# Optimization experiments

Measured on AMD Instinct MI355X. Metric: run time of the kernel, lower is better.

Reference implementation:

```python
import math
import jax, jax.numpy as jnp
import numpy as np

I_DIM = 64
N_MODES = 16
FACTOR = 4
EPS = 1e-5


def group_norm(x, w, b):
    # x: [B, M, N, C] channels-last; torch GroupNorm(C//16, C) over (group_channels, M, N)
    B, M, N, C = x.shape
    g = C // 16
    xr = x.reshape(B, M, N, g, C // g)
    mean = xr.mean(axis=(1, 2, 4), keepdims=True)
    var = xr.var(axis=(1, 2, 4), keepdims=True)
    xr = (xr - mean) * jax.lax.rsqrt(var + EPS)
    return xr.reshape(B, M, N, C) * w + b


def feed_forward(x, res, l1w, l1b, l2w, l2b, g1w, g1b, g2w, g2b, g3w, g3b):
    h = x @ l1w + l1b                      # [B,M,N,C*factor]
    h = group_norm(h, g1w, g1b)            # fork_1
    h = jax.nn.relu(h)
    h = h @ l2w + l2b                      # [B,M,N,C]
    h = group_norm(h, g2w, g2b)            # fork_2
    h = res + h
    h = group_norm(h, g3w, g3b)            # fork_3
    return h


def setup_inputs() -> dict:
    key = jax.random.key(0)
    ks = jax.random.split(key, 20)
    B, M, N, I = 4, 128, 128, I_DIM
    H = I * FACTOR
    z = jax.random.normal(ks[0], (B, 2 * M * N * I, 1), dtype=jnp.float32)
    x = jax.random.normal(ks[1], (B, M * N * I, 1), dtype=jnp.float32)
    # fourier weights [in, out, nm, nm, 2], xavier-ish scale
    fw_scale = math.sqrt(2.0 / (I + I))
    fw1 = jax.random.normal(ks[2], (I, I, N_MODES, N_MODES, 2), dtype=jnp.float32) * fw_scale
    fw2 = jax.random.normal(ks[3], (I, I, N_MODES, N_MODES, 2), dtype=jnp.float32) * fw_scale
    def ff_params(k0):
        kk = jax.random.split(k0, 4)
        return dict(
            l1w=jax.random.normal(kk[0], (I, H), dtype=jnp.float32) * math.sqrt(2.0 / (I + H)),
            l1b=jnp.zeros((H,), jnp.float32),
            l2w=jax.random.normal(kk[1], (H, I), dtype=jnp.float32) * math.sqrt(2.0 / (I + H)),
            l2b=jnp.zeros((I,), jnp.float32),
            g1w=jnp.ones((H,), jnp.float32), g1b=jnp.zeros((H,), jnp.float32),
            g2w=jnp.ones((I,), jnp.float32), g2b=jnp.zeros((I,), jnp.float32),
            g3w=jnp.ones((I,), jnp.float32), g3b=jnp.zeros((I,), jnp.float32),
        )
    bp = ff_params(ks[4])
    fp = ff_params(ks[5])
    out = {"z": z, "x": x, "fw1": fw1, "fw2": fw2}
    for name, p in (("b", bp), ("f", fp)):
        for k, v in p.items():
            out[f"{name}_{k}"] = v
    return out


def reference(z, x, fw1, fw2,
              b_l1w, b_l1b, b_l2w, b_l2b, b_g1w, b_g1b, b_g2w, b_g2b, b_g3w, b_g3b,
              f_l1w, f_l1b, f_l2w, f_l2b, f_g1w, f_g1b, f_g2w, f_g2b, f_g3w, f_g3b):
    I = I_DIM
    nm = N_MODES
    B = x.shape[0]
    M = N = int(math.sqrt(x.shape[1] // I))
    x4 = x.reshape(B, M, N, I)
    z5 = z.reshape(B, 2, M, N, I)
    backcast, forecast = z5[:, 0], z5[:, 1]
    x4 = x4 - backcast
    xc = jnp.transpose(x4, (0, 3, 1, 2))          # [B, I, M, N]
    x_ft = jnp.fft.rfft2(xc, s=(M, N), norm='ortho')  # [B, I, M, N//2+1] complex64
    w1 = fw1[..., 0] + 1j * fw1[..., 1]
    w2 = fw2[..., 0] + 1j * fw2[..., 1]
    top = jnp.einsum('bixy,ioxy->boxy', x_ft[:, :, :nm, :nm], w1)
    bot = jnp.einsum('bixy,ioxy->boxy', x_ft[:, :, -nm:, :nm], w2)
    out_ft = jnp.zeros((B, I, N, M // 2 + 1), dtype=x_ft.dtype)
    out_ft = out_ft.at[:, :, :nm, :nm].set(top).at[:, :, -nm:, :nm].set(bot)
    xo = jnp.fft.irfft2(out_ft, s=(N, M), norm='ortho')  # [B, I, M, N]
    xo = jnp.transpose(xo, (0, 2, 3, 1))                  # [B, M, N, I]
    backcast = feed_forward(xo, backcast, b_l1w, b_l1b, b_l2w, b_l2b,
                            b_g1w, b_g1b, b_g2w, b_g2b, b_g3w, b_g3b)
    forecast = feed_forward(xo, forecast, f_l1w, f_l1b, f_l2w, f_l2b,
                            f_g1w, f_g1b, f_g2w, f_g2b, f_g3w, f_g3b)
    out = jnp.stack([backcast, forecast], axis=1)         # [B, 2, M, N, I]
    return out.reshape(B, 2 * M * N * I, 1)
```

## Files before the change

kernel.cpp:

```cpp
#include <hip/hip_runtime.h>
#include <hip/hip_bf16.h>

typedef __hip_bfloat16 bf16;
typedef __attribute__((ext_vector_type(8))) short short8;
typedef __attribute__((ext_vector_type(4))) float f32x4;

#define PI2 6.283185307179586f
#define EPSV 1e-5f

__device__ __forceinline__ short f2bs(float f){
  bf16 h = __float2bfloat16(f);
  short s; __builtin_memcpy(&s, &h, 2); return s;
}
__device__ __forceinline__ float s2f(short s){
  bf16 h; __builtin_memcpy(&h, &s, 2); return __bfloat162float(h);
}
__device__ __forceinline__ float4 f4add(float4 a, float4 b){ return make_float4(a.x+b.x, a.y+b.y, a.z+b.z, a.w+b.w); }
__device__ __forceinline__ float4 f4sub(float4 a, float4 b){ return make_float4(a.x-b.x, a.y-b.y, a.z-b.z, a.w-b.w); }

__global__ __launch_bounds__(256) void k_prep_ydft(
    const float* __restrict__ x, const float* __restrict__ z,
    const float* __restrict__ fw1, const float* __restrict__ fw2,
    float2* __restrict__ FWT,
    const float* __restrict__ b_l1w, const float* __restrict__ b_l1b,
    const float* __restrict__ b_l2w, const float* __restrict__ b_l2b,
    const float* __restrict__ b_g1w, const float* __restrict__ b_g1b,
    const float* __restrict__ b_g2w, const float* __restrict__ b_g2b,
    const float* __restrict__ b_g3w, const float* __restrict__ b_g3b,
    const float* __restrict__ f_l1w, const float* __restrict__ f_l1b,
    const float* __restrict__ f_l2w, const float* __restrict__ f_l2b,
    const float* __restrict__ f_g1w, const float* __restrict__ f_g1b,
    const float* __restrict__ f_g2w, const float* __restrict__ f_g2b,
    const float* __restrict__ f_g3w, const float* __restrict__ f_g3b,
    short* __restrict__ W1g, short* __restrict__ W2g,
    float2* __restrict__ TWY, float2* __restrict__ TWX,
    float* __restrict__ PB, float* __restrict__ ST,
    float2* __restrict__ Y){
  __shared__ __align__(16) char sm[36864];
  int tid = threadIdx.x;
  int bi = blockIdx.x;
  if(bi < 512){
    float2 (*PQ)[64] = (float2(*)[64])sm;
    float2 (*RS)[64] = (float2(*)[64])(sm + 16384);
    float4 (*twl)[32] = (float4(*)[32])(sm + 32768);
    int b = bi >> 7, m = bi & 127;
    const float4* xp = (const float4*)(x + ((size_t)(b*128 + m)*128)*64);
    const float4* zp = (const float4*)(z + ((size_t)((b*2 + 0)*128 + m)*128)*64);
    int i4 = tid & 15, n0 = tid >> 4;
    #pragma unroll
    for(int it = 0; it < 2; it++){
      int np = n0 + it*16;
      float4 ea = f4sub(xp[np*16 + i4],      zp[np*16 + i4]);
      float4 eb = f4sub(xp[(np+32)*16 + i4], zp[(np+32)*16 + i4]);
      float4 ec = f4sub(xp[(np+64)*16 + i4], zp[(np+64)*16 + i4]);
      float4 ed = f4sub(xp[(np+96)*16 + i4], zp[(np+96)*16 + i4]);
      float4 sac = f4add(ea, ec), sbd = f4add(eb, ed);
      float4 P = f4add(sac, sbd), Q = f4sub(sac, sbd);
      float4 R = f4sub(ea, ec),  S = f4sub(eb, ed);
      *(float4*)&PQ[np][i4*4]     = make_float4(P.x, Q.x, P.y, Q.y);
      *(float4*)&PQ[np][i4*4 + 2] = make_float4(P.z, Q.z, P.w, Q.w);
      *(float4*)&RS[np][i4*4]     = make_float4(R.x, S.x, R.y, S.y);
      *(float4*)&RS[np][i4*4 + 2] = make_float4(R.z, S.z, R.w, S.w);
    }
    {
      int kq2 = tid >> 5, np = tid & 31;
      int ky0 = (kq2 >> 1)*4 + (kq2 & 1)*2;
      float s0, c0, s1, c1;
      sincosf(PI2*(float)((ky0*np) & 127)/128.f, &s0, &c0);
      sincosf(PI2*(float)(((ky0+1)*np) & 127)/128.f, &s1, &c1);
      twl[kq2][np] = make_float4(c0, s0, c1, s1);
    }
    __syncthreads();
    int i = tid & 63, kq = tid >> 6;
    float re[4] = {0,0,0,0}, im[4] = {0,0,0,0};
    for(int np = 0; np < 32; np++){
      float2 pq = PQ[np][i];
      float2 rs = RS[np][i];
      float4 t01 = twl[kq*2][np];
      float4 t23 = twl[kq*2 + 1][np];
      re[0] += pq.x*t01.x;               im[0] -= pq.x*t01.y;
      re[1] += rs.x*t01.z - rs.y*t01.w;  im[1] -= rs.y*t01.z + rs.x*t01.w;
      re[2] += pq.y*t23.x;               im[2] -= pq.y*t23.y;
      re[3] += rs.x*t23.z + rs.y*t23.w;  im[3] += rs.y*t23.z - rs.x*t23.w;
    }
    #pragma unroll
    for(int j = 0; j < 4; j++)
      Y[(((size_t)b*16 + kq*4 + j)*128 + m)*64 + i] = make_float2(re[j], im[j]);
    return;
  }
  if(bi < 1024){
    float (*Ls)[512] = (float(*)[512])sm;
    int bb = bi - 512;
    int arr = bb >> 8, rem = bb & 255;
    int i = rem >> 2, o0 = (rem & 3) * 16;
    const float* src = (arr ? fw2 : fw1) + ((size_t)(i*64 + o0))*512;
    for(int idx = tid; idx < 8192; idx += 256)
      Ls[idx >> 9][idx & 511] = src[idx];
    __syncthreads();
    int kxw = tid >> 4, ky = tid & 15;
    float2* dst = FWT + ((size_t)((arr*16 + kxw)*16 + ky))*4096 + i*64 + o0;
    for(int ol = 0; ol < 16; ol++)
      dst[ol] = make_float2(Ls[ol][tid*2], Ls[ol][tid*2 + 1]);
    return;
  }
  int i = (bi - 1024)*256 + tid;
  if(i < 32768){
    int br = i >> 14, r = i & 16383;
    int fid = r >> 9, lane = (r >> 3) & 63, e = r & 7;
    int hb = fid & 1, t = (fid >> 1) & 3, ch = fid >> 3;
    int l15 = lane & 15, quad = lane >> 4;
    int n = ch*64 + t*16 + l15;
    int k = hb*32 + quad*8 + e;
    const float* src = br ? f_l1w : b_l1w;
    W1g[i] = f2bs(src[k*256 + n]);
    return;
  }
  i -= 32768;
  if(i < 32768){
    int br = i >> 14, r = i & 16383;
    int fid = r >> 9, lane = (r >> 3) & 63, e = r & 7;
    int hb = fid & 1, t = (fid >> 1) & 3, ch = fid >> 3;
    int l15 = lane & 15, quad = lane >> 4;
    int n = t*16 + l15;
    int k = ch*64 + hb*32 + quad*8 + e;
    const float* src = br ? f_l2w : b_l2w;
    W2g[i] = f2bs(src[k*64 + n]);
    return;
  }
  i -= 32768;
  if(i < 2048){
    int ky = i >> 7, n = i & 127;
    float ang = PI2 * (float)((ky*n) & 127) / 128.0f;
    float s, c; sincosf(ang, &s, &c);
    TWY[i] = make_float2(c, s);
    return;
  }
  i -= 2048;
  if(i < 4096){
    int kp = i >> 7, m = i & 127;
    int kx = kp < 16 ? kp : 96 + kp;
    float ang = PI2 * (float)((kx*m) & 127) / 128.0f;
    float s, c; sincosf(ang, &s, &c);
    TWX[i] = make_float2(c, s);
    return;
  }
  i -= 4096;
  if(i < 384){ ST[i] = 0.f; return; }
  i -= 384;
  if(i < 2176){
    int br = i >= 1088; int o = i - br*1088;
    float* pb = PB + br*2048;
    float v;
    if(o < 256)       v = (br ? f_l1b : b_l1b)[o];
    else if(o < 512)  v = (br ? f_g1w : b_g1w)[o-256];
    else if(o < 768)  v = (br ? f_g1b : b_g1b)[o-512];
    else if(o < 832)  v = (br ? f_l2b : b_l2b)[o-768];
    else if(o < 896)  v = (br ? f_g2w : b_g2w)[o-832];
    else if(o < 960)  v = (br ? f_g2b : b_g2b)[o-896];
    else if(o < 1024) v = (br ? f_g3w : b_g3w)[o-960];
    else              v = (br ? f_g3b : b_g3b)[o-1024];
    pb[o] = v;
  }
}

__global__ __launch_bounds__(512) void k_xdft(const float2* __restrict__ Y,
                                              const float2* __restrict__ TWX,
                                              float2* __restrict__ X2,
                                              float* __restrict__ CgZ){
  __shared__ float2 twl[16][64];
  __shared__ float sc[3][128][8];
  int bi = blockIdx.x;
  int b = bi >> 6, ky = (bi >> 2) & 15, half = (bi >> 1) & 1, ih = bi & 1;
  int tid = threadIdx.x;
  int flat = bi*512 + tid;
  if(flat < 16384) CgZ[flat] = 0.f;
  for(int idx = tid; idx < 1024; idx += 512)
    twl[idx >> 6][idx & 63] = TWX[(half*16 + (idx >> 6))*128 + (idx & 63)];
  __syncthreads();
  int i = ih*32 + (tid & 31), grp = (tid >> 5) & 3, mq = tid >> 7;
  const float2* yb = Y + ((size_t)(b*16 + ky)*128)*64 + i;
  float re[4] = {0,0,0,0}, im[4] = {0,0,0,0};
  for(int mi = 0; mi < 16; mi++){
    int mp = mq*16 + mi;
    float2 y1 = yb[(size_t)mp*64];
    float2 y2 = yb[(size_t)(mp + 64)*64];
    float2 ye = make_float2(y1.x + y2.x, y1.y + y2.y);
    float2 yo = make_float2(y1.x - y2.x, y1.y - y2.y);
    float2 t0 = twl[grp*4 + 0][mp];
    float2 t1 = twl[grp*4 + 1][mp];
    float2 t2 = twl[grp*4 + 2][mp];
    float2 t3 = twl[grp*4 + 3][mp];
    re[0] += ye.x*t0.x + ye.y*t0.y;  im[0] += ye.y*t0.x - ye.x*t0.y;
    re[1] += yo.x*t1.x + yo.y*t1.y;  im[1] += yo.y*t1.x - yo.x*t1.y;
    re[2] += ye.x*t2.x + ye.y*t2.y;  im[2] += ye.y*t2.x - ye.x*t2.y;
    re[3] += yo.x*t3.x + yo.y*t3.y;  im[3] += yo.y*t3.x - yo.x*t3.y;
  }
  if(mq){
    int sl = tid & 127;
    #pragma unroll
    for(int j = 0; j < 4; j++){ sc[mq-1][sl][j] = re[j]; sc[mq-1][sl][4 + j] = im[j]; }
  }
  __syncthreads();
  if(!mq){
    const float scn = 1.0f/128.0f;
    #pragma unroll
    for(int j = 0; j < 4; j++){
      float rr = (re[j] + sc[0][tid][j] + sc[1][tid][j] + sc[2][tid][j])*scn;
      float ii = (im[j] + sc[0][tid][4+j] + sc[1][tid][4+j] + sc[2][tid][4+j])*scn;
      int kp = half*16 + grp*4 + j;
      X2[((b*32 + kp)*16 + ky)*64 + i] = make_float2(rr, ii);
    }
  }
}

__global__ __launch_bounds__(512) void k_mix(float2* __restrict__ X2,
                                             const float2* __restrict__ FWT){
  __shared__ float2 Xs[2][4][64];
  __shared__ float sc[3][2][64][8];
  int tid = threadIdx.x;
  {
    int pl = tid >> 8, bq = (tid >> 6) & 3, ii = tid & 63;
    int p = blockIdx.x*2 + pl; int kp = p >> 4, kyy = p & 15;
    Xs[pl][bq][ii] = X2[((bq*32 + kp)*16 + kyy)*64 + ii];
  }
  __syncthreads();
  int o = tid & 63, w = tid >> 6, pl = w >> 2, iq = w & 3;
  int p = blockIdx.x*2 + pl; int kp = p >> 4, ky = p & 15;
  int arr = kp < 16 ? 0 : 1, kxw = kp < 16 ? kp : kp - 16;
  const float2* wp = FWT + ((size_t)((arr*16 + kxw)*16 + ky))*4096;
  float rr[4] = {0,0,0,0}, ii[4] = {0,0,0,0};
  for(int i = iq*16; i < iq*16 + 16; i++){
    float2 wv = wp[i*64 + o];
    #pragma unroll
    for(int b = 0; b < 4; b++){
      float xr = Xs[pl][b][i].x, xi = Xs[pl][b][i].y;
      rr[b] += xr*wv.x - xi*wv.y;
      ii[b] += xr*wv.y + xi*wv.x;
    }
  }
  if(iq){
    #pragma unroll
    for(int b = 0; b < 4; b++){ sc[iq-1][pl][o][b*2] = rr[b]; sc[iq-1][pl][o][b*2 + 1] = ii[b]; }
  }
  __syncthreads();
  if(!iq){
    #pragma unroll
    for(int b = 0; b < 4; b++){
      float r2 = rr[b] + sc[0][pl][o][b*2] + sc[1][pl][o][b*2] + sc[2][pl][o][b*2];
      float i2 = ii[b] + sc[0][pl][o][b*2+1] + sc[1][pl][o][b*2+1] + sc[2][pl][o][b*2+1];
      X2[((b*32 + kp)*16 + ky)*64 + o] = make_float2(r2, i2);
    }
  }
}

__global__ __launch_bounds__(512) void k_inv1scov(const float2* __restrict__ OF,
                                                  const float2* __restrict__ TWX,
                                                  float* __restrict__ Cg,
                                                  float* __restrict__ SX,
                                                  float2* __restrict__ T){
  __shared__ __align__(16) char smu[36864];
  int bi = blockIdx.x;
  int tid = threadIdx.x;
  if(bi < 256){
    float2 (*Fl)[16]  = (float2(*)[16])smu;
    float2 (*twl)[64] = (float2(*)[64])(smu + 4096);
    float  (*sc)[16]  = (float(*)[16])(smu + 20480);
    int b = bi >> 6, ky = (bi >> 2) & 15, oq = bi & 3;
    {
      int kp = tid >> 4, ol = tid & 15;
      Fl[kp][ol] = OF[((b*32 + kp)*16 + ky)*64 + oq*16 + ol];
    }
    for(int idx = tid; idx < 2048; idx += 512){
      int kp = idx >> 6, ml = idx & 63;
      twl[kp][ml] = TWX[kp*128 + ml];
    }
    __syncthreads();
    int ol = tid & 15, mg = (tid >> 4) & 15, kh = tid >> 8;
    float reE[4] = {0,0,0,0}, imE[4] = {0,0,0,0};
    float reO[4] = {0,0,0,0}, imO[4] = {0,0,0,0};
    for(int ip = 0; ip < 8; ip++){
      int kp = kh*16 + ip*2;
      float2 fe = Fl[kp][ol], fo = Fl[kp + 1][ol];
      #pragma unroll
      for(int u = 0; u < 4; u++){
        float2 te = twl[kp][mg*4 + u], to = twl[kp + 1][mg*4 + u];
        reE[u] += fe.x*te.x - fe.y*te.y;
        imE[u] += fe.x*te.y + fe.y*te.x;
        reO[u] += fo.x*to.x - fo.y*to.y;
        imO[u] += fo.x*to.y + fo.y*to.x;
      }
    }
    if(kh){
      int sl = tid & 255;
      #pragma unroll
      for(int u = 0; u < 4; u++){
        sc[sl][u] = reE[u]; sc[sl][4 + u] = imE[u];
        sc[sl][8 + u] = reO[u]; sc[sl][12 + u] = imO[u];
      }
    }
    __syncthreads();
    if(!kh){
      int o = oq*16 + ol;
      #pragma unroll
      for(int u = 0; u < 4; u++){
        float rE = reE[u] + sc[tid][u],     iE = imE[u] + sc[tid][4 + u];
        float rO = reO[u] + sc[tid][8 + u], iO = imO[u] + sc[tid][12 + u];
        int ml = mg*4 + u;
        T[((b*128 + ml)*16 + ky)*64 + o]      = make_float2(rE + rO, iE + iO);
        T[((b*128 + ml + 64)*16 + ky)*64 + o] = make_float2(rE - rO, iE - iO);
      }
    }
    return;
  }
  {
    short (*XT)[264] = (short(*)[264])smu;
    int sb = bi - 256;
    int b = sb >> 2, q = sb & 3;
    const float RT2 = 1.41421356237f, RTH = 0.70710678118f;
    int c0 = (tid & 7)*8;
    #pragma unroll
    for(int it = 0; it < 4; it++){
      int pl = it*64 + (tid >> 3);
      int rg = q*256 + pl;
      int bin = rg >> 1, reim = rg & 1;
      int kp = bin >> 4, ky = bin & 15;
      const float2* base = OF + ((size_t)((b*32 + kp)*16 + ky))*64;
      #pragma unroll
      for(int e = 0; e < 8; e++){
        int i = c0 + e;
        float v;
        if(ky){
          float2 t = base[i];
          v = (reim ? t.y : t.x)*RT2;
        } else if(kp == 0){
          v = reim ? 0.f : base[i].x;
        } else if(kp < 16){
          const float2* mb = OF + ((size_t)((b*32 + (32 - kp))*16))*64;
          float2 t = base[i], u2 = mb[i];
          v = (reim ? 0.5f*(t.y - u2.y) : 0.5f*(t.x + u2.x))*RT2;
        } else if(kp == 16){
          float2 t = base[i];
          v = (reim ? t.y : t.x)*RTH;
        } else {
          v = 0.f;
        }
        XT[i][pl] = f2bs(v);
      }
    }
    if(q == 0 && tid < 64)
      SX[b*64 + tid] = 128.f * OF[((size_t)(b*32)*16)*64 + tid].x;
    __syncthreads();
    int lane = tid & 63, w8 = tid >> 6, wr = w8 & 3, kh = w8 >> 2;
    int l15 = lane & 15, quad = lane >> 4;
    f32x4 acc[4];
    #pragma unroll
    for(int tj = 0; tj < 4; tj++) acc[tj] = (f32x4){0.f,0.f,0.f,0.f};
    for(int kk = kh*4; kk < kh*4 + 4; kk++){
      short8 a = *(const short8*)&XT[wr*16 + l15][kk*32 + quad*8];
      #pragma unroll
      for(int tj = 0; tj < 4; tj++){
        short8 bfr = *(const short8*)&XT[tj*16 + l15][kk*32 + quad*8];
        acc[tj] = __builtin_amdgcn_mfma_f32_16x16x32_bf16(a, bfr, acc[tj], 0, 0, 0);
      }
    }
    float* Cb = Cg + b*4096;
    #pragma unroll
    for(int tj = 0; tj < 4; tj++)
      #pragma unroll
      for(int r = 0; r < 4; r++)
        atomicAdd(&Cb[(wr*16 + quad*4 + r)*64 + tj*16 + l15], acc[tj][r]);
  }
}

__global__ __launch_bounds__(256) void k_stat(const float* __restrict__ Cg,
                                              const float* __restrict__ SX,
                                              const short* __restrict__ W1g,
                                              const float* __restrict__ PB,
                                              float* __restrict__ ST){
  __shared__ float Cl[64][65];
  __shared__ float Wl[16][64];
  __shared__ float sxl[64];
  __shared__ float g2[2];
  int tid = threadIdx.x;
  int br = blockIdx.x >> 6, b = (blockIdx.x >> 4) & 3, g = blockIdx.x & 15;
  const float* Cb = Cg + b*4096;
  for(int u = tid; u < 4096; u += 256) Cl[u >> 6][u & 63] = Cb[u];
  const short* W1 = W1g + br*16384;
  for(int u = tid; u < 1024; u += 256){
    int nl = u >> 6, k = u & 63;
    int n = g*16 + nl;
    int fid = ((n >> 6)*4 + ((n >> 4) & 3))*2 + (k >> 5);
    int lane = ((k >> 3) & 3)*16 + (n & 15);
    Wl[nl][k] = s2f(W1[fid*512 + lane*8 + (k & 7)]);
  }
  if(tid < 64) sxl[tid] = SX[b*64 + tid];
  if(tid < 2) g2[tid] = 0.f;
  __syncthreads();
  int nl = tid >> 4, ic = tid & 15;
  float qa = 0.f, sa = 0.f;
  for(int io = 0; io < 4; io++){
    int i = ic*4 + io;
    float wi = Wl[nl][i];
    float dot = 0.f;
    #pragma unroll 8
    for(int j = 0; j < 64; j++) dot += Cl[i][j]*Wl[nl][j];
    qa += wi*dot;
    sa += wi*sxl[i];
  }
  for(int off = 8; off; off >>= 1){
    qa += __shfl_xor(qa, off);
    sa += __shfl_xor(sa, off);
  }
  if(ic == 0){
    float bn = PB[br*2048 + g*16 + nl];
    float hs = sa + 16384.f*bn;
    float hq = qa + 2.f*bn*sa + 16384.f*bn*bn;
    atomicAdd(&g2[0], hs); atomicAdd(&g2[1], hq);
  }
  __syncthreads();
  if(tid == 0){
    float* S1 = ST + br*192;
    S1[(b*16 + g)*2]     = g2[0];
    S1[(b*16 + g)*2 + 1] = g2[1];
  }
}

__global__ __launch_bounds__(256) void k_inv2(const float2* __restrict__ T,
                                              const float2* __restrict__ TWY,
                                              bf16* __restrict__ XO){
  __shared__ float2 twl[16][64];
  int bi = blockIdx.x;
  int b = bi >> 7, m = bi & 127;
  int tid = threadIdx.x;
  for(int idx = tid; idx < 1024; idx += 256)
    twl[idx >> 6][idx & 63] = TWY[(idx >> 6)*128 + (idx & 63)];
  int o = tid & 63, ng = tid >> 6;
  const float2* tp = T + ((size_t)(b*128 + m)*16)*64 + o;
  float t0a = tp[0].x;
  float ax[15], ay[15];
  #pragma unroll
  for(int u = 0; u < 15; u++){
    float2 v = tp[(u + 1)*64];
    ax[u] = 2.f*v.x; ay[u] = 2.f*v.y;
  }
  __syncthreads();
  const float scn = 1.0f/128.0f;
  bf16* xo = XO + ((size_t)(b*128 + m)*128)*64 + o;
  for(int np = ng*16; np < ng*16 + 16; np++){
    float A = t0a, B = 0.f;
    #pragma unroll
    for(int u = 0; u < 15; u++){
      float2 t = twl[u + 1][np];
      float pr = ax[u]*t.x - ay[u]*t.y;
      if(u & 1) A += pr; else B += pr;
    }
    xo[(size_t)np*64]        = __float2bfloat16((A + B)*scn);
    xo[(size_t)(np + 64)*64] = __float2bfloat16((A - B)*scn);
  }
}

__global__ __launch_bounds__(256, 2) void k_ffmain(const bf16* __restrict__ XO,
                                                   const short* __restrict__ W1g,
                                                   const short* __restrict__ W2g,
                                                   const float* __restrict__ PB,
                                                   const float* __restrict__ ST,
                                                   const float* __restrict__ z,
                                                   float* __restrict__ CS,
                                                   unsigned short* __restrict__ H2){
  __shared__ short Ws1[16384];
  __shared__ short Ws2[16384];
  __shared__ short Hn[64][72];
  __shared__ float mu1[16], rs1[16];
  __shared__ float cs[5][64];
  int tid = threadIdx.x;
  int br = blockIdx.x >> 8, rb = blockIdx.x & 255;
  int r0 = rb << 8, b = rb >> 6;
  const float* pb = PB + br*2048;
  int lane = tid & 63, w = tid >> 6, l15 = lane & 15, quad = lane >> 4;
  int myrow = w*16 + l15;
  short8 a0r[4], a1r[4];
  #pragma unroll
  for(int c = 0; c < 4; c++){
    const short* xop = (const short*)XO + ((size_t)(r0 + c*64 + myrow))*64;
    a0r[c] = *(const short8*)(xop + quad*8);
    a1r[c] = *(const short8*)(xop + 32 + quad*8);
  }
  {
    const uint4* g1 = (const uint4*)(W1g + br*16384);
    const uint4* g2w = (const uint4*)(W2g + br*16384);
    uint4* s1 = (uint4*)Ws1; uint4* s2 = (uint4*)Ws2;
    #pragma unroll
    for(int u = 0; u < 8; u++){
      s1[u*256 + tid] = g1[u*256 + tid];
      s2[u*256 + tid] = g2w[u*256 + tid];
    }
  }
  if(tid < 16){
    const float cnt = 262144.f;
    const float* S1 = ST + br*192;
    float s = S1[(b*16 + tid)*2], q = S1[(b*16 + tid)*2 + 1];
    float mean = s/cnt, var = q/cnt - mean*mean;
    mu1[tid] = mean; rs1[tid] = rsqrtf(fmaxf(var, 0.f) + EPSV);
  }
  {
    float* c1 = &cs[0][0];
    c1[tid] = 0.f;
    if(tid < 64) c1[256 + tid] = 0.f;
  }
  __syncthreads();
  float sh[4]  = {0,0,0,0}, sh2[4] = {0,0,0,0};
  float sz[4]  = {0,0,0,0}, sz2[4] = {0,0,0,0}, shz[4] = {0,0,0,0};
  #pragma unroll
  for(int c = 0; c < 4; c++){
    size_t obase_off = ((size_t)(b*2 + br)*16384 + (r0 & 16383) + c*64)*64;
    const float* zbase = z + obase_off;
    float zr[16];
    #pragma unroll
    for(int t = 0; t < 4; t++)
      #pragma unroll
      for(int r = 0; r < 4; r++)
        zr[t*4 + r] = zbase[(size_t)(w*16 + quad*4 + r)*64 + t*16 + l15];
    f32x4 acc2[4];
    #pragma unroll
    for(int t = 0; t < 4; t++) acc2[t] = (f32x4){0.f,0.f,0.f,0.f};
    for(int ch = 0; ch < 4; ch++){
      #pragma unroll
      for(int t = 0; t < 4; t++){
        int fid = (ch*4 + t)*2;
        short8 b0 = *(const short8*)(Ws1 + fid*512 + lane*8);
        short8 b1 = *(const short8*)(Ws1 + fid*512 + 512 + lane*8);
        f32x4 acc = {0.f,0.f,0.f,0.f};
        acc = __builtin_amdgcn_mfma_f32_16x16x32_bf16(a0r[c], b0, acc, 0, 0, 0);
        acc = __builtin_amdgcn_mfma_f32_16x16x32_bf16(a1r[c], b1, acc, 0, 0, 0);
        int n = ch*64 + t*16 + l15, gi = n >> 4;
        float w1v = pb[256 + n];
        float gwv = w1v * rs1[gi];
        float gbv = (pb[n] - mu1[gi])*rs1[gi]*w1v + pb[512 + n];
        #pragma unroll
        for(int r = 0; r < 4; r++){
          float hv = acc[r]*gwv + gbv;
          hv = hv > 0.f ? hv : 0.f;
          Hn[w*16 + quad*4 + r][t*16 + l15] = f2bs(hv);
        }
      }
      short8 ha0 = *(short8*)&Hn[myrow][quad*8];
      short8 ha1 = *(short8*)&Hn[myrow][32 + quad*8];
      #pragma unroll
      for(int t = 0; t < 4; t++){
        int fid = (ch*4 + t)*2;
        short8 b0 = *(const short8*)(Ws2 + fid*512 + lane*8);
        short8 b1 = *(const short8*)(Ws2 + fid*512 + 512 + lane*8);
        acc2[t] = __builtin_amdgcn_mfma_f32_16x16x32_bf16(ha0, b0, acc2[t], 0, 0, 0);
        acc2[t] = __builtin_amdgcn_mfma_f32_16x16x32_bf16(ha1, b1, acc2[t], 0, 0, 0);
      }
    }
    unsigned short* hbase = H2 + obase_off;
    #pragma unroll
    for(int t = 0; t < 4; t++){
      int col = t*16 + l15;
      float bias2 = pb[768 + col];
      #pragma unroll
      for(int r = 0; r < 4; r++){
        size_t off = (size_t)(w*16 + quad*4 + r)*64 + col;
        float h2 = acc2[t][r] + bias2;
        float zv = zr[t*4 + r];
        hbase[off] = (unsigned short)f2bs(h2);
        sh[t] += h2; sh2[t] += h2*h2;
        sz[t] += zv; sz2[t] += zv*zv; shz[t] += h2*zv;
      }
    }
  }
  #pragma unroll
  for(int t = 0; t < 4; t++){
    float v0 = sh[t], v1 = sh2[t], v2 = sz[t], v3 = sz2[t], v4 = shz[t];
    v0 += __shfl_xor(v0, 16); v0 += __shfl_xor(v0, 32);
    v1 += __shfl_xor(v1, 16); v1 += __shfl_xor(v1, 32);
    v2 += __shfl_xor(v2, 16); v2 += __shfl_xor(v2, 32);
    v3 += __shfl_xor(v3, 16); v3 += __shfl_xor(v3, 32);
    v4 += __shfl_xor(v4, 16); v4 += __shfl_xor(v4, 32);
    if(quad == 0){
      int ch = t*16 + l15;
      atomicAdd(&cs[0][ch], v0); atomicAdd(&cs[1][ch], v1);
      atomicAdd(&cs[2][ch], v2); atomicAdd(&cs[3][ch], v3);
      atomicAdd(&cs[4][ch], v4);
    }
  }
  __syncthreads();
  float* slab = CS + (size_t)blockIdx.x*320;
  const float* c1 = &cs[0][0];
  slab[tid] = c1[tid];
  if(tid < 64) slab[256 + tid] = c1[256 + tid];
}

__global__ __launch_bounds__(256) void k_statB(const float* __restrict__ CS,
                                               const float* __restrict__ PB,
                                               float* __restrict__ CF){
  __shared__ float chs[5][64];
  __shared__ float mu2s[4], rs2s[4], tg[4], tq[4], mu3s[4], rs3s[4];
  int br = blockIdx.x >> 2, b = blockIdx.x & 3;
  int tid = threadIdx.x;
  const float* base = CS + ((size_t)(br*256 + b*64))*320;
  float* c1 = &chs[0][0];
  for(int v = tid; v < 320; v += 256){
    float s = 0.f;
    for(int k = 0; k < 64; k++) s += base[(size_t)k*320 + v];
    c1[v] = s;
  }
  __syncthreads();
  if(tid < 4){
    float s = 0.f, q = 0.f;
    for(int o = tid*16; o < tid*16 + 16; o++){ s += chs[0][o]; q += chs[1][o]; }
    float mean = s/262144.f, var = q/262144.f - mean*mean;
    mu2s[tid] = mean; rs2s[tid] = rsqrtf(fmaxf(var, 0.f) + EPSV);
    tg[tid] = 0.f; tq[tid] = 0.f;
  }
  __syncthreads();
  const float* pb = PB + br*2048;
  if(tid < 64){
    int o = tid, g = o >> 4;
    float w2v = pb[832 + o], b2v = pb[896 + o];
    float gw = w2v*rs2s[g], gb = b2v - mu2s[g]*rs2s[g]*w2v;
    float Sh = chs[0][o], Sh2 = chs[1][o], Sz = chs[2][o], Sz2 = chs[3][o], Shz = chs[4][o];
    float st = gw*Sh + Sz + 16384.f*gb;
    float sq = gw*gw*Sh2 + Sz2 + 16384.f*gb*gb + 2.f*gw*Shz + 2.f*gw*gb*Sh + 2.f*gb*Sz;
    atomicAdd(&tg[g], st); atomicAdd(&tq[g], sq);
  }
  __syncthreads();
  if(tid < 4){
    float mean = tg[tid]/262144.f, var = tq[tid]/262144.f - mean*mean;
    mu3s[tid] = mean; rs3s[tid] = rsqrtf(fmaxf(var, 0.f) + EPSV);
  }
  __syncthreads();
  if(tid < 64){
    int o = tid, g = o >> 4;
    float w2v = pb[832 + o], b2v = pb[896 + o];
    float gw = w2v*rs2s[g], gb = b2v - mu2s[g]*rs2s[g]*w2v;
    float w3v = pb[960 + o], b3v = pb[1024 + o];
    float gw3 = w3v*rs3s[g], gb3 = b3v - mu3s[g]*rs3s[g]*w3v;
    float* cf = CF + (size_t)(br*4 + b)*192;
    cf[o]       = gw*gw3;
    cf[64 + o]  = gw3;
    cf[128 + o] = gb*gw3 + gb3;
  }
}

__global__ __launch_bounds__(256) void k_final(const float* __restrict__ z,
                                               const float* __restrict__ CF,
                                               const unsigned short* __restrict__ H2,
                                               float* __restrict__ out){
  int tid = blockIdx.x*256 + threadIdx.x;
  const float4* z4 = (const float4*)z;
  const float4* cf4 = (const float4*)CF;
  const ushort4* h4 = (const ushort4*)H2;
  float4* o4 = (float4*)out;
  #pragma unroll
  for(int r = 0; r < 8; r++){
    int i4 = r*262144 + tid;
    int s = i4 >> 18;
    int b = s >> 1, br = s & 1;
    int cbase = (br*4 + b)*48 + (i4 & 15);
    float4 a = cf4[cbase], bb = cf4[cbase + 16], g = cf4[cbase + 32];
    ushort4 hu = h4[i4];
    float4 zv = z4[i4];
    o4[i4] = make_float4(s2f((short)hu.x)*a.x + zv.x*bb.x + g.x,
                         s2f((short)hu.y)*a.y + zv.y*bb.y + g.y,
                         s2f((short)hu.z)*a.z + zv.z*bb.z + g.z,
                         s2f((short)hu.w)*a.w + zv.w*bb.w + g.w);
  }
}

extern "C" void kernel_launch(void* const* d_in, const int* in_sizes, int n_in,
                              void* d_out, int out_size, void* d_ws, size_t ws_size,
                              hipStream_t stream){
  const float* z   = (const float*)d_in[0];
  const float* x   = (const float*)d_in[1];
  const float* fw1 = (const float*)d_in[2];
  const float* fw2 = (const float*)d_in[3];
  char* ws = (char*)d_ws;
  float2* Y   = (float2*)(ws + 0);
  float2* X2  = (float2*)(ws + 4194304);
  float2* T   = Y;
  bf16*   XO  = (bf16*)(ws + 5242880);
  float*  ST  = (float*)(ws + 13631488);
  short*  W1g = (short*)(ws + 13633536);
  short*  W2g = (short*)(ws + 13699072);
  float2* TWY = (float2*)(ws + 13764608);
  float2* TWX = (float2*)(ws + 13780992);
  float*  PB  = (float*)(ws + 13813760);
  float2* FWT = (float2*)(ws + 13830144);
  float*  CS  = (float*)(ws + 14878720);
  float*  CF  = (float*)(ws + 15927296);
  unsigned short* H2 = (unsigned short*)(ws + 16777216);
  float*  Cg  = (float*)(ws + 33554432);
  float*  SX  = Cg + 16384;

  const float* p[20];
  for(int i = 0; i < 20; i++) p[i] = (const float*)d_in[4 + i];

  k_prep_ydft<<<1314, 256, 0, stream>>>(x, z, fw1, fw2, FWT,
                                  p[0],p[1],p[2],p[3],p[4],p[5],p[6],p[7],p[8],p[9],
                                  p[10],p[11],p[12],p[13],p[14],p[15],p[16],p[17],p[18],p[19],
                                  W1g, W2g, TWY, TWX, PB, ST, Y);
  k_xdft<<<256, 512, 0, stream>>>(Y, TWX, X2, Cg);
  k_mix<<<256, 512, 0, stream>>>(X2, FWT);
  k_inv1scov<<<272, 512, 0, stream>>>(X2, TWX, Cg, SX, T);
  k_stat<<<128, 256, 0, stream>>>(Cg, SX, W1g, PB, ST);
  k_inv2<<<512, 256, 0, stream>>>(T, TWY, XO);
  k_ffmain<<<512, 256, 0, stream>>>(XO, W1g, W2g, PB, ST, z, CS, H2);
  k_statB<<<8, 256, 0, stream>>>(CS, PB, CF);
  k_final<<<1024, 256, 0, stream>>>(z, CF, H2, (float*)d_out);
}
```

Measured before the change: 240.5 us.

## Merge stat kernels into neighbors and keep FF weights in registers

```diff
diff --git a/kernel.cpp b/kernel.cpp
--- a/kernel.cpp
+++ b/kernel.cpp
@@ -145,8 +145,8 @@
     return;
   }
   i -= 4096;
-  if(i < 384){ ST[i] = 0.f; return; }
-  i -= 384;
+  if(i < 512){ ST[i] = 0.f; return; }
+  i -= 512;
   if(i < 2176){
     int br = i >= 1088; int o = i - br*1088;
     float* pb = PB + br*2048;
@@ -372,90 +372,94 @@
   }
 }
 
-__global__ __launch_bounds__(256) void k_stat(const float* __restrict__ Cg,
-                                              const float* __restrict__ SX,
-                                              const short* __restrict__ W1g,
-                                              const float* __restrict__ PB,
-                                              float* __restrict__ ST){
-  __shared__ float Cl[64][65];
-  __shared__ float Wl[16][64];
-  __shared__ float sxl[64];
-  __shared__ float g2[2];
+__global__ __launch_bounds__(256) void k_inv2stat(const float2* __restrict__ T,
+                                                  const float2* __restrict__ TWY,
+                                                  bf16* __restrict__ XO,
+                                                  const float* __restrict__ Cg,
+                                                  const float* __restrict__ SX,
+                                                  const short* __restrict__ W1g,
+                                                  const float* __restrict__ PB,
+                                                  float* __restrict__ ST){
+  __shared__ __align__(16) char smv[21504];
+  int bi = blockIdx.x;
   int tid = threadIdx.x;
-  int br = blockIdx.x >> 6, b = (blockIdx.x >> 4) & 3, g = blockIdx.x & 15;
-  const float* Cb = Cg + b*4096;
-  for(int u = tid; u < 4096; u += 256) Cl[u >> 6][u & 63] = Cb[u];
-  const short* W1 = W1g + br*16384;
-  for(int u = tid; u < 1024; u += 256){
-    int nl = u >> 6, k = u & 63;
-    int n = g*16 + nl;
-    int fid = ((n >> 6)*4 + ((n >> 4) & 3))*2 + (k >> 5);
-    int lane = ((k >> 3) & 3)*16 + (n & 15);
-    Wl[nl][k] = s2f(W1[fid*512 + lane*8 + (k & 7)]);
-  }
-  if(tid < 64) sxl[tid] = SX[b*64 + tid];
-  if(tid < 2) g2[tid] = 0.f;
-  __syncthreads();
-  int nl = tid >> 4, ic = tid & 15;
-  float qa = 0.f, sa = 0.f;
-  for(int io = 0; io < 4; io++){
-    int i = ic*4 + io;
-    float wi = Wl[nl][i];
-    float dot = 0.f;
-    #pragma unroll 8
-    for(int j = 0; j < 64; j++) dot += Cl[i][j]*Wl[nl][j];
-    qa += wi*dot;
-    sa += wi*sxl[i];
-  }
-  for(int off = 8; off; off >>= 1){
-    qa += __shfl_xor(qa, off);
-    sa += __shfl_xor(sa, off);
-  }
-  if(ic == 0){
-    float bn = PB[br*2048 + g*16 + nl];
-    float hs = sa + 16384.f*bn;
-    float hq = qa + 2.f*bn*sa + 16384.f*bn*bn;
-    atomicAdd(&g2[0], hs); atomicAdd(&g2[1], hq);
-  }
-  __syncthreads();
-  if(tid == 0){
-    float* S1 = ST + br*192;
-    S1[(b*16 + g)*2]     = g2[0];
-    S1[(b*16 + g)*2 + 1] = g2[1];
-  }
-}
-
-__global__ __launch_bounds__(256) void k_inv2(const float2* __restrict__ T,
-                                              const float2* __restrict__ TWY,
-                                              bf16* __restrict__ XO){
-  __shared__ float2 twl[16][64];
-  int bi = blockIdx.x;
-  int b = bi >> 7, m = bi & 127;
-  int tid = threadIdx.x;
-  for(int idx = tid; idx < 1024; idx += 256)
-    twl[idx >> 6][idx & 63] = TWY[(idx >> 6)*128 + (idx & 63)];
-  int o = tid & 63, ng = tid >> 6;
-  const float2* tp = T + ((size_t)(b*128 + m)*16)*64 + o;
-  float t0a = tp[0].x;
-  float ax[15], ay[15];
-  #pragma unroll
-  for(int u = 0; u < 15; u++){
-    float2 v = tp[(u + 1)*64];
-    ax[u] = 2.f*v.x; ay[u] = 2.f*v.y;
-  }
-  __syncthreads();
-  const float scn = 1.0f/128.0f;
-  bf16* xo = XO + ((size_t)(b*128 + m)*128)*64 + o;
-  for(int np = ng*16; np < ng*16 + 16; np++){
-    float A = t0a, B = 0.f;
+  if(bi < 512){
+    float2 (*twl)[64] = (float2(*)[64])smv;
+    int b = bi >> 7, m = bi & 127;
+    for(int idx = tid; idx < 1024; idx += 256)
+      twl[idx >> 6][idx & 63] = TWY[(idx >> 6)*128 + (idx & 63)];
+    int o = tid & 63, ng = tid >> 6;
+    const float2* tp = T + ((size_t)(b*128 + m)*16)*64 + o;
+    float t0a = tp[0].x;
+    float ax[15], ay[15];
     #pragma unroll
     for(int u = 0; u < 15; u++){
-      float2 t = twl[u + 1][np];
-      float pr = ax[u]*t.x - ay[u]*t.y;
-      if(u & 1) A += pr; else B += pr;
-    }
-    xo[(size_t)np*64]        = __float2bfloat16((A + B)*scn);
-    xo[(size_t)(np + 64)*64] = __float2bfloat16((A - B)*scn);
+      float2 v = tp[(u + 1)*64];
+      ax[u] = 2.f*v.x; ay[u] = 2.f*v.y;
+    }
+    __syncthreads();
+    const float scn = 1.0f/128.0f;
+    bf16* xo = XO + ((size_t)(b*128 + m)*128)*64 + o;
+    for(int np = ng*16; np < ng*16 + 16; np++){
+      float A = t0a, B = 0.f;
+      #pragma unroll
+      for(int u = 0; u < 15; u++){
+        float2 t = twl[u + 1][np];
+        float pr = ax[u]*t.x - ay[u]*t.y;
+        if(u & 1) A += pr; else B += pr;
+      }
+      xo[(size_t)np*64]        = __float2bfloat16((A + B)*scn);
+      xo[(size_t)(np + 64)*64] = __float2bfloat16((A - B)*scn);
+    }
+    return;
+  }
+  {
+    float (*Cl)[65] = (float(*)[65])smv;
+    float (*Wl)[64] = (float(*)[64])(smv + 16640);
+    float* sxl = (float*)(smv + 20736);
+    float* g2  = (float*)(smv + 20992);
+    int sb = bi - 512;
+    int br = sb >> 6, b = (sb >> 4) & 3, g = sb & 15;
+    const float* Cb = Cg + b*4096;
+    for(int u = tid; u < 4096; u += 256) Cl[u >> 6][u & 63] = Cb[u];
+    const short* W1 = W1g + br*16384;
+    for(int u = tid; u < 1024; u += 256){
+      int nl = u >> 6, k = u & 63;
+      int n = g*16 + nl;
+      int fid = ((n >> 6)*4 + ((n >> 4) & 3))*2 + (k >> 5);
+      int lane = ((k >> 3) & 3)*16 + (n & 15);
+      Wl[nl][k] = s2f(W1[fid*512 + lane*8 + (k & 7)]);
+    }
+    if(tid < 64) sxl[tid] = SX[b*64 + tid];
+    if(tid < 2) g2[tid] = 0.f;
+    __syncthreads();
+    int nl = tid >> 4, ic = tid & 15;
+    float qa = 0.f, sa = 0.f;
+    for(int io = 0; io < 4; io++){
+      int i = ic*4 + io;
+      float wi = Wl[nl][i];
+      float dot = 0.f;
+      #pragma unroll 8
+      for(int j = 0; j < 64; j++) dot += Cl[i][j]*Wl[nl][j];
+      qa += wi*dot;
+      sa += wi*sxl[i];
+    }
+    for(int off = 8; off; off >>= 1){
+      qa += __shfl_xor(qa, off);
+      sa += __shfl_xor(sa, off);
+    }
+    if(ic == 0){
+      float bn = PB[br*2048 + g*16 + nl];
+      float hs = sa + 16384.f*bn;
+      float hq = qa + 2.f*bn*sa + 16384.f*bn*bn;
+      atomicAdd(&g2[0], hs); atomicAdd(&g2[1], hq);
+    }
+    __syncthreads();
+    if(tid == 0){
+      float* S1 = ST + br*192;
+      S1[(b*16 + g)*2]     = g2[0];
+      S1[(b*16 + g)*2 + 1] = g2[1];
+    }
   }
 }
 
@@ -466,12 +470,14 @@
                                                    const float* __restrict__ ST,
                                                    const float* __restrict__ z,
                                                    float* __restrict__ CS,
-                                                   unsigned short* __restrict__ H2){
-  __shared__ short Ws1[16384];
-  __shared__ short Ws2[16384];
+                                                   unsigned short* __restrict__ H2,
+                                                   unsigned* __restrict__ ticket,
+                                                   float* __restrict__ CF){
   __shared__ short Hn[64][72];
   __shared__ float mu1[16], rs1[16];
   __shared__ float cs[5][64];
+  __shared__ float mu2s[4], rs2s[4], tg[4], tq[4], mu3s[4], rs3s[4];
+  __shared__ unsigned sflag;
   int tid = threadIdx.x;
   int br = blockIdx.x >> 8, rb = blockIdx.x & 255;
   int r0 = rb << 8, b = rb >> 6;
@@ -485,16 +491,6 @@
     a0r[c] = *(const short8*)(xop + quad*8);
     a1r[c] = *(const short8*)(xop + 32 + quad*8);
   }
-  {
-    const uint4* g1 = (const uint4*)(W1g + br*16384);
-    const uint4* g2w = (const uint4*)(W2g + br*16384);
-    uint4* s1 = (uint4*)Ws1; uint4* s2 = (uint4*)Ws2;
-    #pragma unroll
-    for(int u = 0; u < 8; u++){
-      s1[u*256 + tid] = g1[u*256 + tid];
-      s2[u*256 + tid] = g2w[u*256 + tid];
-    }
-  }
   if(tid < 16){
     const float cnt = 262144.f;
     const float* S1 = ST + br*192;
@@ -508,6 +504,51 @@
     if(tid < 64) c1[256 + tid] = 0.f;
   }
   __syncthreads();
+  f32x4 acc2[4][4];
+  #pragma unroll
+  for(int c = 0; c < 4; c++)
+    #pragma unroll
+    for(int t = 0; t < 4; t++) acc2[c][t] = (f32x4){0.f,0.f,0.f,0.f};
+  const short* w1b = W1g + br*16384;
+  const short* w2b = W2g + br*16384;
+  for(int ch = 0; ch < 4; ch++){
+    short8 b0[4], b1[4], c0f[4], c1f[4];
+    float gwv[4], gbv[4];
+    #pragma unroll
+    for(int t = 0; t < 4; t++){
+      int fid = (ch*4 + t)*2;
+      b0[t]  = *(const short8*)(w1b + fid*512 + lane*8);
+      b1[t]  = *(const short8*)(w1b + fid*512 + 512 + lane*8);
+      c0f[t] = *(const short8*)(w2b + fid*512 + lane*8);
+      c1f[t] = *(const short8*)(w2b + fid*512 + 512 + lane*8);
+      int n = ch*64 + t*16 + l15, gi = n >> 4;
+      float w1v = pb[256 + n];
+      gwv[t] = w1v * rs1[gi];
+      gbv[t] = (pb[n] - mu1[gi])*rs1[gi]*w1v + pb[512 + n];
+    }
+    #pragma unroll
+    for(int c = 0; c < 4; c++){
+      #pragma unroll
+      for(int t = 0; t < 4; t++){
+        f32x4 acc = {0.f,0.f,0.f,0.f};
+        acc = __builtin_amdgcn_mfma_f32_16x16x32_bf16(a0r[c], b0[t], acc, 0, 0, 0);
+        acc = __builtin_amdgcn_mfma_f32_16x16x32_bf16(a1r[c], b1[t], acc, 0, 0, 0);
+        #pragma unroll
+        for(int r = 0; r < 4; r++){
+          float hv = acc[r]*gwv[t] + gbv[t];
+          hv = hv > 0.f ? hv : 0.f;
+          Hn[w*16 + quad*4 + r][t*16 + l15] = f2bs(hv);
+        }
+      }
+      short8 ha0 = *(short8*)&Hn[myrow][quad*8];
+      short8 ha1 = *(short8*)&Hn[myrow][32 + quad*8];
+      #pragma unroll
+      for(int t = 0; t < 4; t++){
+        acc2[c][t] = __builtin_amdgcn_mfma_f32_16x16x32_bf16(ha0, c0f[t], acc2[c][t], 0, 0, 0);
+        acc2[c][t] = __builtin_amdgcn_mfma_f32_16x16x32_bf16(ha1, c1f[t], acc2[c][t], 0, 0, 0);
+      }
+    }
+  }
   float sh[4]  = {0,0,0,0}, sh2[4] = {0,0,0,0};
   float sz[4]  = {0,0,0,0}, sz2[4] = {0,0,0,0}, shz[4] = {0,0,0,0};
   #pragma unroll
@@ -520,40 +561,6 @@
       #pragma unroll
       for(int r = 0; r < 4; r++)
         zr[t*4 + r] = zbase[(size_t)(w*16 + quad*4 + r)*64 + t*16 + l15];
-    f32x4 acc2[4];
-    #pragma unroll
-    for(int t = 0; t < 4; t++) acc2[t] = (f32x4){0.f,0.f,0.f,0.f};
-    for(int ch = 0; ch < 4; ch++){
-      #pragma unroll
-      for(int t = 0; t < 4; t++){
-        int fid = (ch*4 + t)*2;
-        short8 b0 = *(const short8*)(Ws1 + fid*512 + lane*8);
-        short8 b1 = *(const short8*)(Ws1 + fid*512 + 512 + lane*8);
-        f32x4 acc = {0.f,0.f,0.f,0.f};
-        acc = __builtin_amdgcn_mfma_f32_16x16x32_bf16(a0r[c], b0, acc, 0, 0, 0);
-        acc = __builtin_amdgcn_mfma_f32_16x16x32_bf16(a1r[c], b1, acc, 0, 0, 0);
-        int n = ch*64 + t*16 + l15, gi = n >> 4;
-        float w1v = pb[256 + n];
-        float gwv = w1v * rs1[gi];
-        float gbv = (pb[n] - mu1[gi])*rs1[gi]*w1v + pb[512 + n];
-        #pragma unroll
-        for(int r = 0; r < 4; r++){
-          float hv = acc[r]*gwv + gbv;
-          hv = hv > 0.f ? hv : 0.f;
-          Hn[w*16 + quad*4 + r][t*16 + l15] = f2bs(hv);
-        }
-      }
-      short8 ha0 = *(short8*)&Hn[myrow][quad*8];
-      short8 ha1 = *(short8*)&Hn[myrow][32 + quad*8];
-      #pragma unroll
-      for(int t = 0; t < 4; t++){
-        int fid = (ch*4 + t)*2;
-        short8 b0 = *(const short8*)(Ws2 + fid*512 + lane*8);
-        short8 b1 = *(const short8*)(Ws2 + fid*512 + 512 + lane*8);
-        acc2[t] = __builtin_amdgcn_mfma_f32_16x16x32_bf16(ha0, b0, acc2[t], 0, 0, 0);
-        acc2[t] = __builtin_amdgcn_mfma_f32_16x16x32_bf16(ha1, b1, acc2[t], 0, 0, 0);
-      }
-    }
     unsigned short* hbase = H2 + obase_off;
     #pragma unroll
     for(int t = 0; t < 4; t++){
@@ -562,7 +569,7 @@
       #pragma unroll
       for(int r = 0; r < 4; r++){
         size_t off = (size_t)(w*16 + quad*4 + r)*64 + col;
-        float h2 = acc2[t][r] + bias2;
+        float h2 = acc2[c][t][r] + bias2;
         float zv = zr[t*4 + r];
         hbase[off] = (unsigned short)f2bs(h2);
         sh[t] += h2; sh2[t] += h2*h2;
@@ -586,61 +593,65 @@
     }
   }
   __syncthreads();
-  float* slab = CS + (size_t)blockIdx.x*320;
-  const float* c1 = &cs[0][0];
-  slab[tid] = c1[tid];
-  if(tid < 64) slab[256 + tid] = c1[256 + tid];
-}
-
-__global__ __launch_bounds__(256) void k_statB(const float* __restrict__ CS,
-                                               const float* __restrict__ PB,
-                                               float* __restrict__ CF){
-  __shared__ float chs[5][64];
-  __shared__ float mu2s[4], rs2s[4], tg[4], tq[4], mu3s[4], rs3s[4];
-  int br = blockIdx.x >> 2, b = blockIdx.x & 3;
-  int tid = threadIdx.x;
-  const float* base = CS + ((size_t)(br*256 + b*64))*320;
-  float* c1 = &chs[0][0];
-  for(int v = tid; v < 320; v += 256){
-    float s = 0.f;
-    for(int k = 0; k < 64; k++) s += base[(size_t)k*320 + v];
-    c1[v] = s;
-  }
+  {
+    float* slab = CS + (size_t)blockIdx.x*320;
+    const float* c1 = &cs[0][0];
+    slab[tid] = c1[tid];
+    if(tid < 64) slab[256 + tid] = c1[256 + tid];
+  }
+  __threadfence();
   __syncthreads();
-  if(tid < 4){
-    float s = 0.f, q = 0.f;
-    for(int o = tid*16; o < tid*16 + 16; o++){ s += chs[0][o]; q += chs[1][o]; }
-    float mean = s/262144.f, var = q/262144.f - mean*mean;
-    mu2s[tid] = mean; rs2s[tid] = rsqrtf(fmaxf(var, 0.f) + EPSV);
-    tg[tid] = 0.f; tq[tid] = 0.f;
-  }
+  if(tid == 0) sflag = atomicAdd(ticket, 1u);
   __syncthreads();
-  const float* pb = PB + br*2048;
-  if(tid < 64){
-    int o = tid, g = o >> 4;
-    float w2v = pb[832 + o], b2v = pb[896 + o];
-    float gw = w2v*rs2s[g], gb = b2v - mu2s[g]*rs2s[g]*w2v;
-    float Sh = chs[0][o], Sh2 = chs[1][o], Sz = chs[2][o], Sz2 = chs[3][o], Shz = chs[4][o];
-    float st = gw*Sh + Sz + 16384.f*gb;
-    float sq = gw*gw*Sh2 + Sz2 + 16384.f*gb*gb + 2.f*gw*Shz + 2.f*gw*gb*Sh + 2.f*gb*Sz;
-    atomicAdd(&tg[g], st); atomicAdd(&tq[g], sq);
-  }
-  __syncthreads();
-  if(tid < 4){
-    float mean = tg[tid]/262144.f, var = tq[tid]/262144.f - mean*mean;
-    mu3s[tid] = mean; rs3s[tid] = rsqrtf(fmaxf(var, 0.f) + EPSV);
-  }
-  __syncthreads();
-  if(tid < 64){
-    int o = tid, g = o >> 4;
-    float w2v = pb[832 + o], b2v = pb[896 + o];
-    float gw = w2v*rs2s[g], gb = b2v - mu2s[g]*rs2s[g]*w2v;
-    float w3v = pb[960 + o], b3v = pb[1024 + o];
-    float gw3 = w3v*rs3s[g], gb3 = b3v - mu3s[g]*rs3s[g]*w3v;
-    float* cf = CF + (size_t)(br*4 + b)*192;
-    cf[o]       = gw*gw3;
-    cf[64 + o]  = gw3;
-    cf[128 + o] = gb*gw3 + gb3;
+  if(sflag == 511){
+    __threadfence();
+    float* chs = &cs[0][0];
+    for(int u = 0; u < 8; u++){
+      int br2 = u >> 2, b2 = u & 3;
+      const float* base2 = CS + ((size_t)(br2*256 + b2*64))*320;
+      __syncthreads();
+      for(int v = tid; v < 320; v += 256){
+        float s = 0.f;
+        for(int k = 0; k < 64; k++) s += base2[(size_t)k*320 + v];
+        chs[v] = s;
+      }
+      __syncthreads();
+      if(tid < 4){
+        float s = 0.f, q = 0.f;
+        for(int o = tid*16; o < tid*16 + 16; o++){ s += chs[o]; q += chs[64 + o]; }
+        float mean = s/262144.f, var = q/262144.f - mean*mean;
+        mu2s[tid] = mean; rs2s[tid] = rsqrtf(fmaxf(var, 0.f) + EPSV);
+        tg[tid] = 0.f; tq[tid] = 0.f;
+      }
+      __syncthreads();
+      const float* pb2 = PB + br2*2048;
+      if(tid < 64){
+        int o = tid, g = o >> 4;
+        float w2v = pb2[832 + o], b2v = pb2[896 + o];
+        float gw = w2v*rs2s[g], gb = b2v - mu2s[g]*rs2s[g]*w2v;
+        float Sh = chs[o], Sh2 = chs[64 + o], Sz = chs[128 + o], Sz2 = chs[192 + o], Shz = chs[256 + o];
+        float st = gw*Sh + Sz + 16384.f*gb;
+        float sq = gw*gw*Sh2 + Sz2 + 16384.f*gb*gb + 2.f*gw*Shz + 2.f*gw*gb*Sh + 2.f*gb*Sz;
+        atomicAdd(&tg[g], st); atomicAdd(&tq[g], sq);
+      }
+      __syncthreads();
+      if(tid < 4){
+        float mean = tg[tid]/262144.f, var = tq[tid]/262144.f - mean*mean;
+        mu3s[tid] = mean; rs3s[tid] = rsqrtf(fmaxf(var, 0.f) + EPSV);
+      }
+      __syncthreads();
+      if(tid < 64){
+        int o = tid, g = o >> 4;
+        float w2v = pb2[832 + o], b2v = pb2[896 + o];
+        float gw = w2v*rs2s[g], gb = b2v - mu2s[g]*rs2s[g]*w2v;
+        float w3v = pb2[960 + o], b3v = pb2[1024 + o];
+        float gw3 = w3v*rs3s[g], gb3 = b3v - mu3s[g]*rs3s[g]*w3v;
+        float* cf = CF + (size_t)(br2*4 + b2)*192;
+        cf[o]       = gw*gw3;
+        cf[64 + o]  = gw3;
+        cf[128 + o] = gb*gw3 + gb3;
+      }
+    }
   }
 }
 
@@ -693,20 +704,19 @@
   unsigned short* H2 = (unsigned short*)(ws + 16777216);
   float*  Cg  = (float*)(ws + 33554432);
   float*  SX  = Cg + 16384;
+  unsigned* ticket = (unsigned*)(ST + 400);
 
   const float* p[20];
   for(int i = 0; i < 20; i++) p[i] = (const float*)d_in[4 + i];
 
-  k_prep_ydft<<<1314, 256, 0, stream>>>(x, z, fw1, fw2, FWT,
+  k_prep_ydft<<<1315, 256, 0, stream>>>(x, z, fw1, fw2, FWT,
                                   p[0],p[1],p[2],p[3],p[4],p[5],p[6],p[7],p[8],p[9],
                                   p[10],p[11],p[12],p[13],p[14],p[15],p[16],p[17],p[18],p[19],
                                   W1g, W2g, TWY, TWX, PB, ST, Y);
   k_xdft<<<256, 512, 0, stream>>>(Y, TWX, X2, Cg);
   k_mix<<<256, 512, 0, stream>>>(X2, FWT);
   k_inv1scov<<<272, 512, 0, stream>>>(X2, TWX, Cg, SX, T);
-  k_stat<<<128, 256, 0, stream>>>(Cg, SX, W1g, PB, ST);
-  k_inv2<<<512, 256, 0, stream>>>(T, TWY, XO);
-  k_ffmain<<<512, 256, 0, stream>>>(XO, W1g, W2g, PB, ST, z, CS, H2);
-  k_statB<<<8, 256, 0, stream>>>(CS, PB, CF);
+  k_inv2stat<<<640, 256, 0, stream>>>(T, TWY, XO, Cg, SX, W1g, PB, ST);
+  k_ffmain<<<512, 256, 0, stream>>>(XO, W1g, W2g, PB, ST, z, CS, H2, ticket, CF);
   k_final<<<1024, 256, 0, stream>>>(z, CF, H2, (float*)d_out);
 }
```

Result: slower. 333.8 us (+38.8%).
